# Performance work log

Measured on AMD Instinct MI355X. Metric: run time of the kernel, lower is better.

The kernel has to match this reference:

```python
import jax, jax.numpy as jnp
import numpy as np

N_NODES = 100000
N_EDGES = 1600000
D = 64


def setup_inputs() -> dict:
    key = jax.random.key(0)
    ks = jax.random.split(key, 9)
    x = jax.random.normal(ks[0], (N_NODES, D), dtype=jnp.float32)
    edge_index = jax.random.randint(ks[1], (2, N_EDGES), 0, N_NODES, dtype=jnp.int64)
    W_self = jax.random.normal(ks[2], (D, D), dtype=jnp.float32) * (D ** -0.5)
    b_self = jax.random.normal(ks[3], (D,), dtype=jnp.float32) * 0.01
    W_neigh = jax.random.normal(ks[4], (D, D), dtype=jnp.float32) * (D ** -0.5)
    b_neigh = jax.random.normal(ks[5], (D,), dtype=jnp.float32) * 0.01
    W_var = jax.random.normal(ks[6], (D, D), dtype=jnp.float32) * (D ** -0.5)
    b_var = jax.random.normal(ks[7], (D,), dtype=jnp.float32) * 0.01
    return {"x": x, "edge_index": edge_index, "W_self": W_self, "b_self": b_self,
            "W_neigh": W_neigh, "b_neigh": b_neigh, "W_var": W_var, "b_var": b_var}


def reference(x, edge_index, W_self, b_self, W_neigh, b_neigh, W_var, b_var):
    N, d = x.shape
    scale = d ** -0.5
    src, dst = edge_index[0], edge_index[1]

    x_src = x[src]                                   # [E, d]
    x_dst = x[dst]                                   # [E, d]

    # reciprocal attention: scatter_softmax over incoming edges of dst
    logits = jnp.sum(x_src * x_dst, axis=-1) * scale               # [E]
    seg_max = jax.ops.segment_max(logits, dst, num_segments=N)     # [N]
    ex = jnp.exp(logits - seg_max[dst])                            # [E]
    denom = jax.ops.segment_sum(ex, dst, num_segments=N)           # [N]
    attn = ex / denom[dst]                                         # [E]

    msg = jax.ops.segment_sum(x_src * attn[:, None], dst, num_segments=N)  # [N, d]

    out = x @ W_self.T + b_self + msg @ W_neigh.T + b_neigh

    # variance via double scatter_mean
    cnt = jax.ops.segment_sum(jnp.ones_like(logits), dst, num_segments=N)
    cnt = jnp.maximum(cnt, 1.0)[:, None]                           # [N, 1]
    msg_mean = jax.ops.segment_sum(x_src, dst, num_segments=N) / cnt
    diff_sq = (x_src - msg_mean[dst]) ** 2                         # [E, d]
    var = jax.ops.segment_sum(diff_sq, dst, num_segments=N) / cnt  # [N, d]

    out = out + var @ W_var.T + b_var
    return out
```

## Files before the change

### kernel.cpp

```cpp
#include <hip/hip_runtime.h>


static inline size_t ws_align(size_t x) { return (x + 255) & ~size_t(255); }

typedef __attribute__((ext_vector_type(8))) short bf16x8;
typedef __attribute__((ext_vector_type(4))) float f32x4;
typedef __attribute__((ext_vector_type(2))) float f32x2;

#define ECHUNK 4096
#define CAP    5120
#define ESC    0.18033688f

__device__ __forceinline__ unsigned short f2bf(float f) {
    unsigned u = __builtin_bit_cast(unsigned, f);
    u += 0x7FFFu + ((u >> 16) & 1u);
    return (unsigned short)(u >> 16);
}
__device__ __forceinline__ float bfhi(int d) {
    return __builtin_bit_cast(float, (unsigned)d & 0xFFFF0000u);
}
__device__ __forceinline__ float bflo(int d) {
    return __builtin_bit_cast(float, (unsigned)d << 16);
}

__device__ __forceinline__ float fast_exp2(float t) {
#if __has_builtin(__builtin_amdgcn_exp2f)
    return __builtin_amdgcn_exp2f(t);
#else
    return exp2f(t);
#endif
}

template <int CTRL>
__device__ __forceinline__ float dpp_radd(float t) {
    int v = __builtin_amdgcn_update_dpp(0, __builtin_bit_cast(int, t),
                                        CTRL, 0xF, 0xF, true);
    return t + __builtin_bit_cast(float, v);
}
__device__ __forceinline__ float row16_sum(float t) {
    t = dpp_radd<0xB1>(t);
    t = dpp_radd<0x4E>(t);
    t = dpp_radd<0x124>(t);
    t = dpp_radd<0x128>(t);
    return t;
}

__device__ __forceinline__ float combine4(float t) {
    t += __shfl_xor(t, 16, 64);
    t += __shfl_xor(t, 32, 64);
    return t;
}

__global__ void __launch_bounds__(512) build_kernel(
        const float* __restrict__ x, unsigned short* __restrict__ xb,
        const int* __restrict__ ei, int* __restrict__ gcnt,
        int* __restrict__ tmp, int E, int n4, int nb1) {
    __shared__ int cnt[512];
    __shared__ int base[512];
    int tid = threadIdx.x;
    for (int k = tid; k < nb1; k += 512) cnt[k] = 0;
    int stride = gridDim.x * 512;
    for (int i = blockIdx.x * 512 + tid; i < n4; i += stride) {
        float4 v = ((const float4*)x)[i];
        ushort4 hh; hh.x = f2bf(v.x); hh.y = f2bf(v.y); hh.z = f2bf(v.z); hh.w = f2bf(v.w);
        ((ushort4*)xb)[i] = hh;
    }
    __syncthreads();
    const int* dstp = ei + E;
    int cbase = blockIdx.x * ECHUNK;
    int dcache[ECHUNK / 512];
    int scache[ECHUNK / 512];
    #pragma unroll
    for (int k = 0; k < ECHUNK / 512; ++k) {
        int e = cbase + k * 512 + tid;
        int d = (e < E) ? dstp[e] : -1;
        dcache[k] = d;
        scache[k] = (e < E) ? ei[e] : 0;
        if (d >= 0) atomicAdd(&cnt[d >> 8], 1);
    }
    __syncthreads();
    for (int k = tid; k < nb1; k += 512) {
        int c = cnt[k];
        base[k] = c ? atomicAdd(&gcnt[k], c) : 0;
        cnt[k] = 0;
    }
    __syncthreads();
    #pragma unroll
    for (int k = 0; k < ECHUNK / 512; ++k) {
        int dst = dcache[k];
        if (dst >= 0) {
            int b = dst >> 8;
            int r = base[b] + atomicAdd(&cnt[b], 1);
            if (r < CAP)
                tmp[b * CAP + r] = (scache[k] << 8) | (dst & 255);
        }
    }
}

__global__ void __launch_bounds__(512) fsort_kernel(
        const int* __restrict__ tmp, const int* __restrict__ gcnt,
        int* __restrict__ srcs, int* __restrict__ rs, int* __restrict__ re,
        int N, int nb1) {
    __shared__ int cnt[256], sc[256], lofs[256];
    __shared__ int stage[CAP];
    int b = blockIdx.x, tid = threadIdx.x;
    int start = b * CAP;
    int seg = min(gcnt[b], CAP);

    if (tid < 256) cnt[tid] = 0;
    for (int k = tid; k < seg; k += 512) stage[k] = tmp[start + k];
    __syncthreads();
    for (int k = tid; k < seg; k += 512) atomicAdd(&cnt[stage[k] & 255], 1);
    __syncthreads();
    int c = (tid < 256) ? cnt[tid] : 0;
    if (tid < 256) sc[tid] = c;
    __syncthreads();
    for (int off = 1; off < 256; off <<= 1) {
        int u = (tid < 256 && tid >= off) ? sc[tid - off] : 0;
        __syncthreads();
        if (tid < 256) sc[tid] += u;
        __syncthreads();
    }
    if (tid < 256) {
        int excl = sc[tid] - c;
        int node = b * 256 + tid;
        if (node < N) { rs[node] = start + excl; re[node] = start + excl + c; }
        lofs[tid] = start + excl;
    }
    __syncthreads();
    for (int k = tid; k < seg; k += 512) {
        int v = stage[k];
        int pos = atomicAdd(&lofs[v & 255], 1);
        srcs[pos] = v >> 8;
    }
}

__global__ void __launch_bounds__(256) node_gather_kernel(
        const unsigned short* __restrict__ xb,
        const int* __restrict__ rs, const int* __restrict__ re,
        const int* __restrict__ srcs,
        unsigned short* __restrict__ msgvar, int N) {
    int w = (blockIdx.x * blockDim.x + threadIdx.x) >> 6;
    if (w >= N) return;
    int lane = threadIdx.x & 63;
    int q = lane & 15;
    int g = lane >> 4;
    int s = rs[w], e = re[w];
    const int2* xb2 = (const int2*)xb;
    int2 dn = xb2[(size_t)w * 16 + q];
    f32x2 esc2 = {ESC, ESC};
    f32x2 xn01 = {bflo(dn.x), bfhi(dn.x)}, xn23 = {bflo(dn.y), bfhi(dn.y)};
    xn01 *= esc2; xn23 *= esc2;
    float den = 0.f;
    f32x2 sxa = {0,0}, sxb = {0,0}, ssqa = {0,0}, ssqb = {0,0},
          smea = {0,0}, smeb = {0,0};

    auto compute = [&](int2 d) {
        f32x2 a = {bflo(d.x), bfhi(d.x)};
        f32x2 b = {bflo(d.y), bfhi(d.y)};
        f32x2 dp = a * xn01 + b * xn23;
        float t = row16_sum(dp.x + dp.y);
        float ex = fast_exp2(t);
        f32x2 ex2 = {ex, ex};
        den += ex;
        sxa += a;           sxb += b;
        ssqa += a * a;      ssqb += b * b;
        smea += ex2 * a;    smeb += ex2 * b;
    };

    for (int base = s; base < e; base += 64) {
        int cnt = min(e - base, 64);
        int idx = srcs[base + min(lane, cnt - 1)];
        int p = 0;
        int2 da, db;
        if (p + 8 <= cnt) {
            int ra = __shfl(idx, p + g, 64);
            int rb = __shfl(idx, p + 4 + g, 64);
            da = xb2[(size_t)ra * 16 + q];
            db = xb2[(size_t)rb * 16 + q];
        }
        for (; p + 16 <= cnt; p += 8) {
            int ra1 = __shfl(idx, p + 8 + g, 64);
            int rb1 = __shfl(idx, p + 12 + g, 64);
            int2 da1 = xb2[(size_t)ra1 * 16 + q];
            int2 db1 = xb2[(size_t)rb1 * 16 + q];
            compute(da);
            compute(db);
            da = da1; db = db1;
        }
        if (p + 8 <= cnt) {
            compute(da);
            compute(db);
            p += 8;
        }
        for (; p < cnt; p += 4) {
            float wt = (p + g < cnt) ? 1.f : 0.f;
            int r = __shfl(idx, min(p + g, cnt - 1), 64);
            int2 d = xb2[(size_t)r * 16 + q];
            f32x2 a = {bflo(d.x), bfhi(d.x)};
            f32x2 b = {bflo(d.y), bfhi(d.y)};
            f32x2 dp = a * xn01 + b * xn23;
            float t = row16_sum(dp.x + dp.y);
            float ex = fast_exp2(t) * wt;
            f32x2 wt2 = {wt, wt}, ex2 = {ex, ex};
            f32x2 wa = a * wt2, wb = b * wt2;
            den += ex;
            sxa += wa;          sxb += wb;
            ssqa += wa * a;     ssqb += wb * b;
            smea += ex2 * a;    smeb += ex2 * b;
        }
    }
    den    = combine4(den);
    sxa.x  = combine4(sxa.x);  sxa.y  = combine4(sxa.y);
    sxb.x  = combine4(sxb.x);  sxb.y  = combine4(sxb.y);
    ssqa.x = combine4(ssqa.x); ssqa.y = combine4(ssqa.y);
    ssqb.x = combine4(ssqb.x); ssqb.y = combine4(ssqb.y);
    smea.x = combine4(smea.x); smea.y = combine4(smea.y);
    smeb.x = combine4(smeb.x); smeb.y = combine4(smeb.y);
    if (lane < 16) {
        float inv = 1.f / fmaxf((float)(e - s), 1.f);
        float invden = (den > 0.f) ? (1.f / den) : 0.f;
        float m0 = sxa.x * inv, m1 = sxa.y * inv, m2 = sxb.x * inv, m3 = sxb.y * inv;
        ushort4 hm, hv;
        hm.x = f2bf(smea.x * invden); hm.y = f2bf(smea.y * invden);
        hm.z = f2bf(smeb.x * invden); hm.w = f2bf(smeb.y * invden);
        hv.x = f2bf(ssqa.x * inv - m0 * m0); hv.y = f2bf(ssqa.y * inv - m1 * m1);
        hv.z = f2bf(ssqb.x * inv - m2 * m2); hv.w = f2bf(ssqb.y * inv - m3 * m3);
        *(ushort4*)&msgvar[(size_t)w * 128 + 4 * q]      = hm;
        *(ushort4*)&msgvar[(size_t)w * 128 + 64 + 4 * q] = hv;
    }
}

__global__ void __launch_bounds__(256) gemm_kernel(
        const unsigned short* __restrict__ xb, const unsigned short* __restrict__ msgvar,
        const float* __restrict__ Ws, const float* __restrict__ bs,
        const float* __restrict__ Wn, const float* __restrict__ bn,
        const float* __restrict__ Wv, const float* __restrict__ bv,
        float* __restrict__ out, int N) {
    __shared__ unsigned short As[64 * 200];
    int tid = threadIdx.x;
    int lane = tid & 63;
    int wv = tid >> 6;
    int j = lane & 15, quad = lane >> 4;
    int jg = wv * 16 + j;

    const float* Wm0[3] = {Ws, Wn, Wv};
    bf16x8 bfrag[6];
    #pragma unroll
    for (int ks = 0; ks < 6; ++ks) {
        const float* W = Wm0[ks >> 1];
        int k0 = (ks & 1) * 32 + quad * 8;
        const float4* p = (const float4*)(W + (size_t)jg * 64 + k0);
        float4 a = p[0], b = p[1];
        bf16x8 f;
        f[0] = (short)f2bf(a.x); f[1] = (short)f2bf(a.y);
        f[2] = (short)f2bf(a.z); f[3] = (short)f2bf(a.w);
        f[4] = (short)f2bf(b.x); f[5] = (short)f2bf(b.y);
        f[6] = (short)f2bf(b.z); f[7] = (short)f2bf(b.w);
        bfrag[ks] = f;
    }
    float bias = bs[jg] + bn[jg] + bv[jg];

    #pragma unroll
    for (int t = 0; t < 2; ++t) {
        int nbase = blockIdx.x * 128 + t * 64;
        #pragma unroll
        for (int i = 0; i < 4; ++i) {
            int idx = i * 256 + tid;
            int row = idx >> 4, c = idx & 15;
            int n = min(nbase + row, N - 1);
            ushort4 h = ((const ushort4*)(xb + (size_t)n * 64))[c];
            *(ushort4*)&As[row * 200 + c * 4] = h;
        }
        #pragma unroll
        for (int i = 0; i < 8; ++i) {
            int idx = i * 256 + tid;
            int row = idx >> 5, c = idx & 31;
            int n = min(nbase + row, N - 1);
            ushort4 h = ((const ushort4*)(msgvar + (size_t)n * 128))[c];
            *(ushort4*)&As[row * 200 + 64 + c * 4] = h;
        }
        __syncthreads();

        f32x4 acc[4];
        #pragma unroll
        for (int nt = 0; nt < 4; ++nt) {
            acc[nt][0] = bias; acc[nt][1] = bias; acc[nt][2] = bias; acc[nt][3] = bias;
        }
        #pragma unroll
        for (int nt = 0; nt < 4; ++nt) {
            #pragma unroll
            for (int ks = 0; ks < 6; ++ks) {
                const bf16x8* ap = (const bf16x8*)&As[(nt * 16 + j) * 200 + ks * 32 + quad * 8];
                acc[nt] = __builtin_amdgcn_mfma_f32_16x16x32_bf16(*ap, bfrag[ks], acc[nt], 0, 0, 0);
            }
        }
        #pragma unroll
        for (int nt = 0; nt < 4; ++nt) {
            #pragma unroll
            for (int r = 0; r < 4; ++r) {
                int node = nbase + nt * 16 + quad * 4 + r;
                if (node < N) out[(size_t)node * 64 + jg] = acc[nt][r];
            }
        }
        __syncthreads();
    }
}

extern "C" void kernel_launch(void* const* d_in, const int* in_sizes, int n_in,
                              void* d_out, int out_size, void* d_ws, size_t ws_size,
                              hipStream_t stream) {
    const float* x  = (const float*)d_in[0];
    const int*   ei = (const int*)d_in[1];
    const float* Ws = (const float*)d_in[2];
    const float* bs = (const float*)d_in[3];
    const float* Wn = (const float*)d_in[4];
    const float* bn = (const float*)d_in[5];
    const float* Wv = (const float*)d_in[6];
    const float* bv = (const float*)d_in[7];
    float* out = (float*)d_out;

    int N  = in_sizes[0] / 64;
    int E  = in_sizes[1] / 2;
    int nblk = (E + ECHUNK - 1) / ECHUNK;
    int nb1  = (N + 255) >> 8;

    char* wsp = (char*)d_ws;
    size_t off = 0;
    int* gcnt   = (int*)(wsp + off); off += ws_align((size_t)nb1 * 4);
    int* rs     = (int*)(wsp + off); off += ws_align((size_t)N * 4);
    int* re     = (int*)(wsp + off); off += ws_align((size_t)N * 4);
    int* tmp    = (int*)(wsp + off); off += ws_align((size_t)nb1 * CAP * 4);
    int* srcs   = (int*)(wsp + off); off += ws_align((size_t)nb1 * CAP * 4);
    unsigned short* msgvar = (unsigned short*)(wsp + off); off += ws_align((size_t)N * 128 * 2);
    unsigned short* xb     = (unsigned short*)(wsp + off); off += ws_align((size_t)N * 64 * 2);

    int n4 = N * 16;
    hipMemsetAsync(gcnt, 0, (size_t)nb1 * 4, stream);
    build_kernel<<<nblk, 512, 0, stream>>>(x, xb, ei, gcnt, tmp, E, n4, nb1);
    fsort_kernel<<<nb1, 512, 0, stream>>>(tmp, gcnt, srcs, rs, re, N, nb1);
    node_gather_kernel<<<((size_t)N * 64 + 255) / 256, 256, 0, stream>>>(xb, rs, re, srcs, msgvar, N);
    gemm_kernel<<<(N + 127) / 128, 256, 0, stream>>>(xb, msgvar, Ws, bs, Wn, bn, Wv, bv, out, N);
}
```

Measured before the change: 191.5 us.

## Process two destination nodes per wavefront in node gather kernel

```diff
diff --git a/kernel.cpp b/kernel.cpp
--- a/kernel.cpp
+++ b/kernel.cpp
@@ -45,9 +45,8 @@
     return t;
 }
 
-__device__ __forceinline__ float combine4(float t) {
+__device__ __forceinline__ float combine2(float t) {
     t += __shfl_xor(t, 16, 64);
-    t += __shfl_xor(t, 32, 64);
     return t;
 }
 
@@ -140,14 +139,20 @@
         const int* __restrict__ rs, const int* __restrict__ re,
         const int* __restrict__ srcs,
         unsigned short* __restrict__ msgvar, int N) {
-    int w = (blockIdx.x * blockDim.x + threadIdx.x) >> 6;
-    if (w >= N) return;
+    int pair = (blockIdx.x * blockDim.x + threadIdx.x) >> 6;
+    if (pair * 2 >= N) return;
     int lane = threadIdx.x & 63;
-    int q = lane & 15;
-    int g = lane >> 4;
-    int s = rs[w], e = re[w];
+    int half = lane >> 5;
+    int hl = lane & 31;
+    int q = hl & 15;
+    int g = hl >> 4;
+    int w = pair * 2 + half;
+    bool valid = (w < N);
+    int s = 0, e = 0;
+    if (valid) { s = rs[w]; e = re[w]; }
     const int2* xb2 = (const int2*)xb;
-    int2 dn = xb2[(size_t)w * 16 + q];
+    int wc = min(w, N - 1);
+    int2 dn = xb2[(size_t)wc * 16 + q];
     f32x2 esc2 = {ESC, ESC};
     f32x2 xn01 = {bflo(dn.x), bfhi(dn.x)}, xn23 = {bflo(dn.y), bfhi(dn.y)};
     xn01 *= esc2; xn23 *= esc2;
@@ -168,34 +173,34 @@
         smea += ex2 * a;    smeb += ex2 * b;
     };
 
-    for (int base = s; base < e; base += 64) {
-        int cnt = min(e - base, 64);
-        int idx = srcs[base + min(lane, cnt - 1)];
+    for (int base = s; base < e; base += 32) {
+        int cnt = min(e - base, 32);
+        int idx = srcs[base + min(hl, cnt - 1)];
         int p = 0;
         int2 da, db;
-        if (p + 8 <= cnt) {
-            int ra = __shfl(idx, p + g, 64);
-            int rb = __shfl(idx, p + 4 + g, 64);
+        if (p + 4 <= cnt) {
+            int ra = __shfl(idx, p + g, 32);
+            int rb = __shfl(idx, p + 2 + g, 32);
             da = xb2[(size_t)ra * 16 + q];
             db = xb2[(size_t)rb * 16 + q];
         }
-        for (; p + 16 <= cnt; p += 8) {
-            int ra1 = __shfl(idx, p + 8 + g, 64);
-            int rb1 = __shfl(idx, p + 12 + g, 64);
+        for (; p + 8 <= cnt; p += 4) {
+            int ra1 = __shfl(idx, p + 4 + g, 32);
+            int rb1 = __shfl(idx, p + 6 + g, 32);
             int2 da1 = xb2[(size_t)ra1 * 16 + q];
             int2 db1 = xb2[(size_t)rb1 * 16 + q];
             compute(da);
             compute(db);
             da = da1; db = db1;
         }
-        if (p + 8 <= cnt) {
+        if (p + 4 <= cnt) {
             compute(da);
             compute(db);
-            p += 8;
-        }
-        for (; p < cnt; p += 4) {
+            p += 4;
+        }
+        for (; p < cnt; p += 2) {
             float wt = (p + g < cnt) ? 1.f : 0.f;
-            int r = __shfl(idx, min(p + g, cnt - 1), 64);
+            int r = __shfl(idx, min(p + g, cnt - 1), 32);
             int2 d = xb2[(size_t)r * 16 + q];
             f32x2 a = {bflo(d.x), bfhi(d.x)};
             f32x2 b = {bflo(d.y), bfhi(d.y)};
@@ -210,14 +215,14 @@
             smea += ex2 * a;    smeb += ex2 * b;
         }
     }
-    den    = combine4(den);
-    sxa.x  = combine4(sxa.x);  sxa.y  = combine4(sxa.y);
-    sxb.x  = combine4(sxb.x);  sxb.y  = combine4(sxb.y);
-    ssqa.x = combine4(ssqa.x); ssqa.y = combine4(ssqa.y);
-    ssqb.x = combine4(ssqb.x); ssqb.y = combine4(ssqb.y);
-    smea.x = combine4(smea.x); smea.y = combine4(smea.y);
-    smeb.x = combine4(smeb.x); smeb.y = combine4(smeb.y);
-    if (lane < 16) {
+    den    = combine2(den);
+    sxa.x  = combine2(sxa.x);  sxa.y  = combine2(sxa.y);
+    sxb.x  = combine2(sxb.x);  sxb.y  = combine2(sxb.y);
+    ssqa.x = combine2(ssqa.x); ssqa.y = combine2(ssqa.y);
+    ssqb.x = combine2(ssqb.x); ssqb.y = combine2(ssqb.y);
+    smea.x = combine2(smea.x); smea.y = combine2(smea.y);
+    smeb.x = combine2(smeb.x); smeb.y = combine2(smeb.y);
+    if (valid && hl < 16) {
         float inv = 1.f / fmaxf((float)(e - s), 1.f);
         float invden = (den > 0.f) ? (1.f / den) : 0.f;
         float m0 = sxa.x * inv, m1 = sxa.y * inv, m2 = sxb.x * inv, m3 = sxb.y * inv;
@@ -339,6 +344,8 @@
     hipMemsetAsync(gcnt, 0, (size_t)nb1 * 4, stream);
     build_kernel<<<nblk, 512, 0, stream>>>(x, xb, ei, gcnt, tmp, E, n4, nb1);
     fsort_kernel<<<nb1, 512, 0, stream>>>(tmp, gcnt, srcs, rs, re, N, nb1);
-    node_gather_kernel<<<((size_t)N * 64 + 255) / 256, 256, 0, stream>>>(xb, rs, re, srcs, msgvar, N);
+    int npair = (N + 1) / 2;
+    node_gather_kernel<<<((size_t)npair * 64 + 255) / 256, 256, 0, stream>>>(
+        xb, rs, re, srcs, msgvar, N);
     gemm_kernel<<<(N + 127) / 128, 256, 0, stream>>>(xb, msgvar, Ws, bs, Wn, bn, Wv, bv, out, N);
 }
```

After: 178.1 us. -7.0%, faster.
